# Performance work log

Measured on AMD Instinct MI355X. Metric: run time of the kernel, lower is better.

The kernel has to match this reference:

```python
import jax, jax.numpy as jnp
import numpy as np

MIDC = 128
HEADS = 8
HEADC = MIDC // HEADS
EPS = 1e-5


def setup_inputs() -> dict:
    key = jax.random.key(0)
    ks = jax.random.split(key, 7)
    B, C, H, W = 8, MIDC, 128, 128
    x = jax.random.normal(ks[0], (B, C, H, W), dtype=jnp.float32)
    s = 1.0 / np.sqrt(C)
    qkv_w = jax.random.normal(ks[1], (3 * C, C), dtype=jnp.float32) * s
    qkv_b = jnp.zeros((3 * C,), dtype=jnp.float32)
    o1_w = jax.random.normal(ks[2], (C, C), dtype=jnp.float32) * s
    o1_b = jnp.zeros((C,), dtype=jnp.float32)
    o2_w = jax.random.normal(ks[3], (C, C), dtype=jnp.float32) * s
    o2_b = jnp.zeros((C,), dtype=jnp.float32)
    kln_w = jnp.ones((HEADS, 1, HEADC), dtype=jnp.float32)
    kln_b = jnp.zeros((HEADS, 1, HEADC), dtype=jnp.float32)
    vln_w = jnp.ones((HEADS, 1, HEADC), dtype=jnp.float32)
    vln_b = jnp.zeros((HEADS, 1, HEADC), dtype=jnp.float32)
    return {"x": x, "qkv_w": qkv_w, "qkv_b": qkv_b, "o1_w": o1_w, "o1_b": o1_b,
            "o2_w": o2_w, "o2_b": o2_b, "kln_w": kln_w, "kln_b": kln_b,
            "vln_w": vln_w, "vln_b": vln_b}


def _layernorm(t, w, b):
    # torch LayerNorm clone: mean/std over last dim, std uses ddof=1 (unbiased)
    mean = t.mean(-1, keepdims=True)
    std = jnp.std(t, axis=-1, ddof=1, keepdims=True)
    return w * ((t - mean) / (std + EPS)) + b


def reference(x, qkv_w, qkv_b, o1_w, o1_b, o2_w, o2_b, kln_w, kln_b, vln_w, vln_b):
    B, C, H, W = x.shape
    N = H * W
    bias0 = x
    # 1x1 conv == pointwise linear over channels
    xf = x.transpose(0, 2, 3, 1).reshape(B, N, C)              # [B, N, C]
    qkv = xf @ qkv_w.T + qkv_b                                 # [B, N, 3C]
    qkv = qkv.reshape(B, N, HEADS, 3 * HEADC).transpose(0, 2, 1, 3)  # [B, h, N, 3d]
    q, k, v = jnp.split(qkv, 3, axis=-1)                       # each [B, h, N, d]
    k = _layernorm(k, kln_w, kln_b)
    v = _layernorm(v, vln_w, vln_b)
    kv = jnp.einsum('bhnd,bhne->bhde', k, v) / N               # [B, h, d, d]
    av = jnp.einsum('bhnd,bhde->bhne', q, kv)                  # [B, h, N, d]
    av = av.transpose(0, 2, 1, 3).reshape(B, H, W, C)
    ret = av.transpose(0, 3, 1, 2) + bias0                     # [B, C, H, W]
    # o_proj1 -> GELU -> o_proj2, residual
    rf = ret.transpose(0, 2, 3, 1)                             # [B, H, W, C]
    h1 = jax.nn.gelu(rf @ o1_w.T + o1_b, approximate=False)
    h2 = h1 @ o2_w.T + o2_b
    return h2.transpose(0, 3, 1, 2) + bias0
```

## Files before the change

kernel.cpp:

```cpp
#include <hip/hip_runtime.h>
#include <hip/hip_bf16.h>

#define LN_EPS 1e-5f

typedef __bf16 bf16x8 __attribute__((ext_vector_type(8)));
typedef float  f32x4  __attribute__((ext_vector_type(4)));
typedef unsigned short u16;
typedef unsigned int u32;

__device__ __forceinline__ u16 f2bf(float f) {
    __bf16 b = (__bf16)f;
    return __builtin_bit_cast(u16, b);
}
__device__ __forceinline__ bf16x8 zero8() {
    bf16x8 v;
#pragma unroll
    for (int j = 0; j < 8; j++) v[j] = (__bf16)0.f;
    return v;
}
__device__ __forceinline__ float gelu_f(float v) {
    float t = v * fmaf(v * v, 0.0713548162726f, 1.5957691216057f);
    return v / (1.f + __expf(-t));
}

__global__ __launch_bounds__(256) void prep_kernel(
    const float* __restrict__ qkv_w, const float* __restrict__ o1_w,
    const float* __restrict__ o2_w, u16* __restrict__ wq,
    u16* __restrict__ o1f, u16* __restrict__ o2f) {
    int i = blockIdx.x * 256 + threadIdx.x;
    if (i >= 81920) return;
    int j = i;
    const float* src;
    u16* dst;
    if (j < 49152) { src = qkv_w; dst = wq; }
    else if (j < 65536) { j -= 49152; src = o1_w; dst = o1f; }
    else { j -= 65536; src = o2_w; dst = o2f; }
    int jj = j & 7;
    int l  = (j >> 3) & 63;
    int s  = (j >> 9) & 3;
    int t  = j >> 11;
    int outc = t * 16 + (l & 15);
    int k    = s * 32 + ((l >> 4) & 3) * 8 + jj;
    dst[j] = f2bf(src[outc * 128 + k]);
}

__global__ __launch_bounds__(512, 6) void k1(
    const float* __restrict__ x, const u16* __restrict__ wq,
    const float* __restrict__ qkv_b,
    const float* __restrict__ klw, const float* __restrict__ klb,
    const float* __restrict__ vlw, const float* __restrict__ vlb,
    u16* __restrict__ q_ws, float* __restrict__ part) {
    __shared__ __align__(16) char Rbuf[36864];
    u16* x_a  = (u16*)Rbuf;
    u16* kv_s = (u16*)Rbuf;
    u16* kT   = (u16*)Rbuf;
    u16* vT   = (u16*)Rbuf + 9216;

    const int tid  = threadIdx.x;
    const int lane = tid & 63;
    const int wv   = tid >> 6;
    const int stripe = wv >> 1;
    const int half   = wv & 1;
    const int bid  = blockIdx.x;
    const int b    = bid >> 8;
    const int n0   = (bid & 255) * 64;

    {
        int cw  = tid & 63;
        int sub = tid >> 6;
        const float* p0 = x + ((size_t)(b * 128 + 2 * cw)) * 16384 + n0 + sub * 8;
        const float* p1 = p0 + 16384;
        float4 a0 = ((const float4*)p0)[0], a1 = ((const float4*)p0)[1];
        float4 c0 = ((const float4*)p1)[0], c1 = ((const float4*)p1)[1];
        float av[8] = {a0.x, a0.y, a0.z, a0.w, a1.x, a1.y, a1.z, a1.w};
        float cv[8] = {c0.x, c0.y, c0.z, c0.w, c1.x, c1.y, c1.z, c1.w};
        u32* dst = (u32*)x_a;
#pragma unroll
        for (int j = 0; j < 8; j++)
            dst[(sub * 8 + j) * 68 + cw] = (u32)f2bf(av[j]) | ((u32)f2bf(cv[j]) << 16);
    }
    __syncthreads();

    const int m16  = stripe * 16;
    const int l15  = lane & 15;
    const int quad = lane >> 4;

    bf16x8 af[4];
#pragma unroll
    for (int s = 0; s < 4; s++)
        af[s] = *(const bf16x8*)&x_a[(m16 + l15) * 136 + s * 32 + quad * 8];
    __syncthreads();

    const int tb = half * 12;
#pragma unroll
    for (int hh = 0; hh < 4; hh++) {
        const int tq = tb + 3 * hh;
        f32x4 aq  = (f32x4){0.f, 0.f, 0.f, 0.f};
        f32x4 ak  = (f32x4){0.f, 0.f, 0.f, 0.f};
        f32x4 avv = (f32x4){0.f, 0.f, 0.f, 0.f};
#pragma unroll
        for (int s = 0; s < 4; s++) {
            bf16x8 bq = *(const bf16x8*)(wq + (size_t)(((tq + 0) * 4 + s) * 64 + lane) * 8);
            bf16x8 bk = *(const bf16x8*)(wq + (size_t)(((tq + 1) * 4 + s) * 64 + lane) * 8);
            bf16x8 bv = *(const bf16x8*)(wq + (size_t)(((tq + 2) * 4 + s) * 64 + lane) * 8);
            aq  = __builtin_amdgcn_mfma_f32_16x16x32_bf16(af[s], bq, aq, 0, 0, 0);
            ak  = __builtin_amdgcn_mfma_f32_16x16x32_bf16(af[s], bk, ak, 0, 0, 0);
            avv = __builtin_amdgcn_mfma_f32_16x16x32_bf16(af[s], bv, avv, 0, 0, 0);
        }
        const int h = half * 4 + hh;
        float biasq = qkv_b[(tq + 0) * 16 + l15];
        float biask = qkv_b[(tq + 1) * 16 + l15];
        float biasv = qkv_b[(tq + 2) * 16 + l15];
#pragma unroll
        for (int r = 0; r < 4; r++) {
            int row = m16 + quad * 4 + r;
            q_ws[((size_t)(b * 16384) + n0 + row) * 128 + h * 16 + l15] = f2bf(aq[r] + biasq);
            kv_s[row * 264 + h * 32 + l15]      = f2bf(ak[r] + biask);
            kv_s[row * 264 + h * 32 + 16 + l15] = f2bf(avv[r] + biasv);
        }
    }
    __syncthreads();

    const int hL = __builtin_amdgcn_readfirstlane(wv);
    const u16* rowp = &kv_s[lane * 264 + hL * 32];
    bf16x8 rk0 = *(const bf16x8*)(rowp);
    bf16x8 rk1 = *(const bf16x8*)(rowp + 8);
    bf16x8 rv0 = *(const bf16x8*)(rowp + 16);
    bf16x8 rv1 = *(const bf16x8*)(rowp + 24);
    __syncthreads();

    {
        float kf[16], vf[16];
#pragma unroll
        for (int j = 0; j < 8; j++) {
            kf[j] = (float)rk0[j]; kf[8 + j] = (float)rk1[j];
            vf[j] = (float)rv0[j]; vf[8 + j] = (float)rv1[j];
        }
        float ksum = 0.f, ksq = 0.f, vsum = 0.f, vsq = 0.f;
#pragma unroll
        for (int d = 0; d < 16; d++) {
            ksum += kf[d]; ksq = fmaf(kf[d], kf[d], ksq);
            vsum += vf[d]; vsq = fmaf(vf[d], vf[d], vsq);
        }
        float km = ksum * (1.f / 16.f);
        float kvar = (ksq - 16.f * km * km) * (1.f / 15.f);
        kvar = kvar < 0.f ? 0.f : kvar;
        float kinv = 1.f / (sqrtf(kvar) + LN_EPS);
        float vm = vsum * (1.f / 16.f);
        float vvar = (vsq - 16.f * vm * vm) * (1.f / 15.f);
        vvar = vvar < 0.f ? 0.f : vvar;
        float vinv = 1.f / (sqrtf(vvar) + LN_EPS);
        const float* kwp = klw + hL * 16; const float* kbp = klb + hL * 16;
        const float* vwp = vlw + hL * 16; const float* vbp = vlb + hL * 16;
#pragma unroll
        for (int d = 0; d < 16; d++) {
            kT[(hL * 16 + d) * 72 + lane] = f2bf(fmaf((kf[d] - km) * kinv, kwp[d], kbp[d]));
            vT[(hL * 16 + d) * 72 + lane] = f2bf(fmaf((vf[d] - vm) * vinv, vwp[d], vbp[d]));
        }
    }
    __syncthreads();

    {
        const u16* ka = &kT[(hL * 16 + l15) * 72 + quad * 8];
        const u16* vb = &vT[(hL * 16 + l15) * 72 + quad * 8];
        bf16x8 A0 = *(const bf16x8*)(ka);
        bf16x8 A1 = *(const bf16x8*)(ka + 32);
        bf16x8 B0 = *(const bf16x8*)(vb);
        bf16x8 B1 = *(const bf16x8*)(vb + 32);
        f32x4 kv = __builtin_amdgcn_mfma_f32_16x16x32_bf16(A0, B0, (f32x4){0.f,0.f,0.f,0.f}, 0, 0, 0);
        kv = __builtin_amdgcn_mfma_f32_16x16x32_bf16(A1, B1, kv, 0, 0, 0);
        ((f32x4*)part)[(size_t)(bid * 8 + hL) * 64 + lane] = kv;
    }
}

__global__ __launch_bounds__(256) void k_red(const float* __restrict__ part,
                                             u16* __restrict__ kvf) {
    int gid = blockIdx.x * 256 + threadIdx.x;
    int b = gid >> 11, e = gid & 2047;
    int h = e >> 8, dk = (e >> 4) & 15, dv = e & 15;
    size_t base = (size_t)h * 256 + (size_t)(((dk >> 2) * 16 + dv) * 4 + (dk & 3));
    float s = 0.f;
    for (int t = 0; t < 256; t++)
        s += part[((size_t)(b * 256 + t)) * 2048 + base];
    kvf[(size_t)(b * 8 + h) * 256 + (dk >> 3) * 128 + dv * 8 + (dk & 7)] =
        f2bf(s * (1.f / 16384.f));
}

__global__ __launch_bounds__(256, 5) void k2(
    const float* __restrict__ x, const u16* __restrict__ q_ws,
    const u16* __restrict__ kvf, const u16* __restrict__ o1f,
    const u16* __restrict__ o2f, const float* __restrict__ o1_b,
    const float* __restrict__ o2_b, float* __restrict__ out) {
    __shared__ u16 a_s[32 * 136];
    __shared__ float x_s[128 * 36];

    const int tid  = threadIdx.x;
    const int lane = tid & 63;
    const int wv   = tid >> 6;
    const int stripe = wv >> 1;
    const int half   = wv & 1;
    const int bid  = blockIdx.x;
    const int b    = bid >> 9;
    const int n0   = (bid & 511) * 32;

    {
        int row = tid >> 3, seg = tid & 7;
        const uint4* qs = (const uint4*)(q_ws + ((size_t)(b * 16384) + n0 + row) * 128 + seg * 16);
        uint4* qd = (uint4*)&a_s[row * 136 + seg * 16];
        qd[0] = qs[0];
        qd[1] = qs[1];

        int c = tid >> 1, nh = (tid & 1) * 16;
        const float4* xs = (const float4*)(x + ((size_t)(b * 128 + c)) * 16384 + n0 + nh);
        float4* xd = (float4*)&x_s[c * 36 + nh];
#pragma unroll
        for (int i = 0; i < 4; i++) xd[i] = xs[i];
    }
    __syncthreads();

    const int m16  = stripe * 16;
    const int l15  = lane & 15;
    const int quad = lane >> 4;
    const bool act = quad < 2;

    float retv[4][4];
#pragma unroll
    for (int hh = 0; hh < 4; hh++) {
        int h = half * 4 + hh;
        bf16x8 afr = zero8(), bfr = zero8();
        if (act) {
            afr = *(const bf16x8*)&a_s[(m16 + l15) * 136 + h * 16 + quad * 8];
            bfr = *(const bf16x8*)(kvf + (size_t)(b * 8 + h) * 256 + quad * 128 + l15 * 8);
        }
        f32x4 acc = __builtin_amdgcn_mfma_f32_16x16x32_bf16(
            afr, bfr, (f32x4){0.f,0.f,0.f,0.f}, 0, 0, 0);
#pragma unroll
        for (int r = 0; r < 4; r++)
            retv[hh][r] = acc[r] + x_s[(h * 16 + l15) * 36 + m16 + quad * 4 + r];
    }
#pragma unroll
    for (int hh = 0; hh < 4; hh++)
#pragma unroll
        for (int r = 0; r < 4; r++)
            a_s[(m16 + quad * 4 + r) * 136 + (half * 4 + hh) * 16 + l15] = f2bf(retv[hh][r]);
    __syncthreads();

    bf16x8 af2[4];
#pragma unroll
    for (int s = 0; s < 4; s++)
        af2[s] = *(const bf16x8*)&a_s[(m16 + l15) * 136 + s * 32 + quad * 8];
    f32x4 acc2[4];
#pragma unroll
    for (int t = 0; t < 4; t++) acc2[t] = (f32x4){0.f,0.f,0.f,0.f};
#pragma unroll
    for (int tt = 0; tt < 4; tt++) {
        int t = half * 4 + tt;
#pragma unroll
        for (int s = 0; s < 4; s++) {
            bf16x8 bf = *(const bf16x8*)(o1f + (size_t)((t * 4 + s) * 64 + lane) * 8);
            acc2[tt] = __builtin_amdgcn_mfma_f32_16x16x32_bf16(af2[s], bf, acc2[tt], 0, 0, 0);
        }
    }
    float g[4][4];
#pragma unroll
    for (int tt = 0; tt < 4; tt++) {
        float bb = o1_b[(half * 4 + tt) * 16 + l15];
#pragma unroll
        for (int r = 0; r < 4; r++)
            g[tt][r] = gelu_f(acc2[tt][r] + bb);
    }
    __syncthreads();
#pragma unroll
    for (int tt = 0; tt < 4; tt++)
#pragma unroll
        for (int r = 0; r < 4; r++)
            a_s[(m16 + quad * 4 + r) * 136 + (half * 4 + tt) * 16 + l15] = f2bf(g[tt][r]);
    __syncthreads();

#pragma unroll
    for (int s = 0; s < 4; s++)
        af2[s] = *(const bf16x8*)&a_s[(m16 + l15) * 136 + s * 32 + quad * 8];
#pragma unroll
    for (int t = 0; t < 4; t++) acc2[t] = (f32x4){0.f,0.f,0.f,0.f};
#pragma unroll
    for (int tt = 0; tt < 4; tt++) {
        int t = half * 4 + tt;
#pragma unroll
        for (int s = 0; s < 4; s++) {
            bf16x8 bf = *(const bf16x8*)(o2f + (size_t)((t * 4 + s) * 64 + lane) * 8);
            acc2[tt] = __builtin_amdgcn_mfma_f32_16x16x32_bf16(af2[s], bf, acc2[tt], 0, 0, 0);
        }
    }
#pragma unroll
    for (int tt = 0; tt < 4; tt++) {
        int t = half * 4 + tt;
        float bb = o2_b[t * 16 + l15];
#pragma unroll
        for (int r = 0; r < 4; r++) {
            int row = m16 + quad * 4 + r;
            int col = t * 16 + l15;
            x_s[col * 36 + row] = acc2[tt][r] + bb + x_s[col * 36 + row];
        }
    }
    __syncthreads();

    {
        int c = tid >> 1, nh = (tid & 1) * 16;
        float4* dst = (float4*)(out + ((size_t)(b * 128 + c)) * 16384 + n0 + nh);
        const float4* sv = (const float4*)&x_s[c * 36 + nh];
#pragma unroll
        for (int i = 0; i < 4; i++) dst[i] = sv[i];
    }
}

extern "C" void kernel_launch(void* const* d_in, const int* in_sizes, int n_in,
                              void* d_out, int out_size, void* d_ws, size_t ws_size,
                              hipStream_t stream) {
    (void)in_sizes; (void)n_in; (void)out_size; (void)ws_size;
    const float* x     = (const float*)d_in[0];
    const float* qkv_w = (const float*)d_in[1];
    const float* qkv_b = (const float*)d_in[2];
    const float* o1_w  = (const float*)d_in[3];
    const float* o1_b  = (const float*)d_in[4];
    const float* o2_w  = (const float*)d_in[5];
    const float* o2_b  = (const float*)d_in[6];
    const float* klw   = (const float*)d_in[7];
    const float* klb   = (const float*)d_in[8];
    const float* vlw   = (const float*)d_in[9];
    const float* vlb   = (const float*)d_in[10];
    float* outp = (float*)d_out;

    char* ws = (char*)d_ws;
    u16*   kvf  = (u16*)(ws);
    u16*   wq   = (u16*)(ws + 32768);
    u16*   o1f  = (u16*)(ws + 131072);
    u16*   o2f  = (u16*)(ws + 163840);
    float* part = (float*)(ws + 196608);
    u16*   q_ws = (u16*)(ws + 196608 + 16777216);

    prep_kernel<<<320, 256, 0, stream>>>(qkv_w, o1_w, o2_w, wq, o1f, o2f);
    k1<<<2048, 512, 0, stream>>>(x, wq, qkv_b, klw, klb, vlw, vlb, q_ws, part);
    k_red<<<64, 256, 0, stream>>>(part, kvf);
    k2<<<4096, 256, 0, stream>>>(x, q_ws, kvf, o1f, o2f, o1_b, o2_b, outp);
}
```

Baseline: 221.5 us.

## Store Q in MFMA fragment layout, stage via LDS, and split k_red reduction

```diff
diff --git a/kernel.cpp b/kernel.cpp
--- a/kernel.cpp
+++ b/kernel.cpp
@@ -50,11 +50,12 @@
     const float* __restrict__ klw, const float* __restrict__ klb,
     const float* __restrict__ vlw, const float* __restrict__ vlb,
     u16* __restrict__ q_ws, float* __restrict__ part) {
-    __shared__ __align__(16) char Rbuf[36864];
+    __shared__ __align__(16) char Rbuf[51200];
     u16* x_a  = (u16*)Rbuf;
     u16* kv_s = (u16*)Rbuf;
+    u16* q_s  = (u16*)(Rbuf + 33792);
     u16* kT   = (u16*)Rbuf;
-    u16* vT   = (u16*)Rbuf + 9216;
+    u16* vT   = (u16*)(Rbuf + 18432);
 
     const int tid  = threadIdx.x;
     const int lane = tid & 63;
@@ -114,13 +115,26 @@
 #pragma unroll
         for (int r = 0; r < 4; r++) {
             int row = m16 + quad * 4 + r;
-            q_ws[((size_t)(b * 16384) + n0 + row) * 128 + h * 16 + l15] = f2bf(aq[r] + biasq);
+            q_s[row * 136 + h * 16 + l15]       = f2bf(aq[r] + biasq);
             kv_s[row * 264 + h * 32 + l15]      = f2bf(ak[r] + biask);
             kv_s[row * 264 + h * 32 + 16 + l15] = f2bf(avv[r] + biasv);
         }
     }
     __syncthreads();
 
+    {
+#pragma unroll
+        for (int p = 0; p < 2; p++) {
+            int c = tid + p * 512;
+            int lane_c = c & 63;
+            int s  = (c >> 6) & 3;
+            int tl = c >> 8;
+            int row = tl * 16 + (lane_c & 15);
+            const uint4* src = (const uint4*)&q_s[row * 136 + s * 32 + (lane_c >> 4) * 8];
+            size_t gtile = (size_t)b * 1024 + (n0 >> 4) + tl;
+            *(uint4*)(q_ws + gtile * 2048 + s * 512 + lane_c * 8) = *src;
+        }
+    }
     const int hL = __builtin_amdgcn_readfirstlane(wv);
     const u16* rowp = &kv_s[lane * 264 + hL * 32];
     bf16x8 rk0 = *(const bf16x8*)(rowp);
@@ -175,15 +189,28 @@
 
 __global__ __launch_bounds__(256) void k_red(const float* __restrict__ part,
                                              u16* __restrict__ kvf) {
-    int gid = blockIdx.x * 256 + threadIdx.x;
-    int b = gid >> 11, e = gid & 2047;
+    __shared__ float red[256];
+    int tid = threadIdx.x;
+    int b  = blockIdx.x >> 5;
+    int eg = blockIdx.x & 31;
+    int el = tid & 63;
+    int tchunk = tid >> 6;
+    int e = eg * 64 + el;
     int h = e >> 8, dk = (e >> 4) & 15, dv = e & 15;
-    size_t base = (size_t)h * 256 + (size_t)(((dk >> 2) * 16 + dv) * 4 + (dk & 3));
+    size_t off = (size_t)h * 256 + (size_t)(((dk >> 2) * 16 + dv) * 4 + (dk & 3));
     float s = 0.f;
-    for (int t = 0; t < 256; t++)
-        s += part[((size_t)(b * 256 + t)) * 2048 + base];
-    kvf[(size_t)(b * 8 + h) * 256 + (dk >> 3) * 128 + dv * 8 + (dk & 7)] =
-        f2bf(s * (1.f / 16384.f));
+#pragma unroll 8
+    for (int t = tchunk * 64; t < tchunk * 64 + 64; t++)
+        s += part[((size_t)(b * 256 + t)) * 2048 + off];
+    red[tid] = s;
+    __syncthreads();
+    if (tid < 64) {
+        float total = red[tid] + red[tid + 64] + red[tid + 128] + red[tid + 192];
+        int e2 = eg * 64 + tid;
+        int h2 = e2 >> 8, dk2 = (e2 >> 4) & 15, dv2 = e2 & 15;
+        kvf[(size_t)(b * 8 + h2) * 256 + (dk2 >> 3) * 128 + dv2 * 8 + (dk2 & 7)] =
+            f2bf(total * (1.f / 16384.f));
+    }
 }
 
 __global__ __launch_bounds__(256, 5) void k2(
@@ -203,46 +230,47 @@
     const int b    = bid >> 9;
     const int n0   = (bid & 511) * 32;
 
-    {
-        int row = tid >> 3, seg = tid & 7;
-        const uint4* qs = (const uint4*)(q_ws + ((size_t)(b * 16384) + n0 + row) * 128 + seg * 16);
-        uint4* qd = (uint4*)&a_s[row * 136 + seg * 16];
-        qd[0] = qs[0];
-        qd[1] = qs[1];
-
-        int c = tid >> 1, nh = (tid & 1) * 16;
-        const float4* xs = (const float4*)(x + ((size_t)(b * 128 + c)) * 16384 + n0 + nh);
-        float4* xd = (float4*)&x_s[c * 36 + nh];
-#pragma unroll
-        for (int i = 0; i < 4; i++) xd[i] = xs[i];
-    }
-    __syncthreads();
-
     const int m16  = stripe * 16;
     const int l15  = lane & 15;
     const int quad = lane >> 4;
     const bool act = quad < 2;
 
-    float retv[4][4];
+    bf16x8 qf[4], kvb[4];
+    {
+        size_t gtile = (size_t)b * 1024 + (n0 >> 4) + stripe;
+#pragma unroll
+        for (int hh = 0; hh < 4; hh++) {
+            int h = half * 4 + hh;
+            if (act) {
+                int laneq = ((h & 1) * 2 + quad) * 16 + l15;
+                qf[hh]  = *(const bf16x8*)(q_ws + gtile * 2048 + (h >> 1) * 512 + laneq * 8);
+                kvb[hh] = *(const bf16x8*)(kvf + (size_t)(b * 8 + h) * 256 + quad * 128 + l15 * 8);
+            } else {
+                qf[hh] = zero8(); kvb[hh] = zero8();
+            }
+        }
+    }
+
+    {
+        int c = tid >> 1, nh = (tid & 1) * 16;
+        const float4* xs = (const float4*)(x + ((size_t)(b * 128 + c)) * 16384 + n0 + nh);
+        float4* xd = (float4*)&x_s[c * 36 + nh];
+#pragma unroll
+        for (int i = 0; i < 4; i++) xd[i] = xs[i];
+    }
+    __syncthreads();
+
 #pragma unroll
     for (int hh = 0; hh < 4; hh++) {
         int h = half * 4 + hh;
-        bf16x8 afr = zero8(), bfr = zero8();
-        if (act) {
-            afr = *(const bf16x8*)&a_s[(m16 + l15) * 136 + h * 16 + quad * 8];
-            bfr = *(const bf16x8*)(kvf + (size_t)(b * 8 + h) * 256 + quad * 128 + l15 * 8);
-        }
         f32x4 acc = __builtin_amdgcn_mfma_f32_16x16x32_bf16(
-            afr, bfr, (f32x4){0.f,0.f,0.f,0.f}, 0, 0, 0);
-#pragma unroll
-        for (int r = 0; r < 4; r++)
-            retv[hh][r] = acc[r] + x_s[(h * 16 + l15) * 36 + m16 + quad * 4 + r];
-    }
-#pragma unroll
-    for (int hh = 0; hh < 4; hh++)
-#pragma unroll
-        for (int r = 0; r < 4; r++)
-            a_s[(m16 + quad * 4 + r) * 136 + (half * 4 + hh) * 16 + l15] = f2bf(retv[hh][r]);
+            qf[hh], kvb[hh], (f32x4){0.f,0.f,0.f,0.f}, 0, 0, 0);
+#pragma unroll
+        for (int r = 0; r < 4; r++) {
+            float rv = acc[r] + x_s[(h * 16 + l15) * 36 + m16 + quad * 4 + r];
+            a_s[(m16 + quad * 4 + r) * 136 + h * 16 + l15] = f2bf(rv);
+        }
+    }
     __syncthreads();
 
     bf16x8 af2[4];
@@ -340,6 +368,6 @@
 
     prep_kernel<<<320, 256, 0, stream>>>(qkv_w, o1_w, o2_w, wq, o1f, o2f);
     k1<<<2048, 512, 0, stream>>>(x, wq, qkv_b, klw, klb, vlw, vlb, q_ws, part);
-    k_red<<<64, 256, 0, stream>>>(part, kvf);
+    k_red<<<256, 256, 0, stream>>>(part, kvf);
     k2<<<4096, 256, 0, stream>>>(x, q_ws, kvf, o1f, o2f, o1_b, o2_b, outp);
 }
```

After: 207.0 us. 6.5% less time.
